# Optimization experiments

Measured on AMD Instinct MI355X. Metric: run time of the kernel, lower is better.

## Reference

```python
import jax, jax.numpy as jnp
import numpy as np
import math

B, T, C, H = 2, 2048, 1024, 16
HD = C // H  # head_dim = 64
SCALE = 1.0 / math.sqrt(HD)


def _e8_head_dirs(n_heads: int) -> np.ndarray:
    # Type-1 E8 roots in original generation order: (+-1 at i, +-1 at j), i<j,
    # sign order (-1,-1),(-1,1),(1,-1),(1,1); then L2-normalized (norm sqrt(2)).
    roots = []
    for i in range(8):
        for j in range(i + 1, 8):
            for si in (-1.0, 1.0):
                for sj in (-1.0, 1.0):
                    r = np.zeros(8, dtype=np.float32)
                    r[i] = si
                    r[j] = sj
                    roots.append(r)
    roots = np.stack(roots)  # [112, 8], first n_heads used
    roots = roots / np.linalg.norm(roots, axis=1, keepdims=True)
    return roots[:n_heads]


def setup_inputs() -> dict:
    key = jax.random.key(0)
    k1, k2, k3, k4 = jax.random.split(key, 4)
    x = jax.random.normal(k1, (B, T, C), dtype=jnp.float32)
    # nn.Linear-style init scale
    w_qkv = jax.random.normal(k2, (C, 3 * C), dtype=jnp.float32) * (1.0 / math.sqrt(C))
    w_out = jax.random.normal(k3, (C, C), dtype=jnp.float32) * (1.0 / math.sqrt(C))
    head_scales = jax.random.normal(k4, (H,), dtype=jnp.float32) * 0.1
    head_dirs = jnp.asarray(_e8_head_dirs(H))  # [H, 8] buffer (not trained)
    return {"x": x, "w_qkv": w_qkv, "w_out": w_out,
            "head_scales": head_scales, "head_dirs": head_dirs}


def reference(x, w_qkv, w_out, head_scales, head_dirs):
    Bx, Tx, Cx = x.shape
    qkv = (x @ w_qkv).reshape(Bx, Tx, 3, H, HD)
    qkv = jnp.transpose(qkv, (2, 0, 3, 1, 4))  # [3, B, H, T, HD]
    q, k, v = qkv[0], qkv[1], qkv[2]
    scores = jnp.einsum('bhqd,bhkd->bhqk', q, k) * SCALE  # [B,H,T,T]
    causal = jnp.tril(jnp.ones((Tx, Tx), dtype=bool))
    scores = jnp.where(causal[None, None], scores, -jnp.inf)
    # E8 geometric bias: rank-1 per-head bias from projections onto root dirs
    q_proj = jnp.einsum('bhtd,hd->bht', q[..., :8], head_dirs)
    k_proj = jnp.einsum('bhtd,hd->bht', k[..., :8], head_dirs)
    geo_bias = q_proj[..., :, None] * k_proj[..., None, :]  # [B,H,T,T]
    scores = scores + head_scales[None, :, None, None] * geo_bias
    attn = jax.nn.softmax(scores, axis=-1)
    out = jnp.einsum('bhqk,bhkd->bhqd', attn, v)  # [B,H,T,HD]
    out = jnp.transpose(out, (0, 2, 1, 3)).reshape(Bx, Tx, Cx)
    return out @ w_out
```

## Files before the change

kernel.cpp:

```cpp
#include <hip/hip_runtime.h>
#include <stdint.h>


typedef float f32x4 __attribute__((ext_vector_type(4)));
typedef unsigned short u16x8 __attribute__((ext_vector_type(8)));
typedef unsigned short u16x4 __attribute__((ext_vector_type(4)));
typedef unsigned int u32x2 __attribute__((ext_vector_type(2)));
typedef __bf16 bf16x8 __attribute__((ext_vector_type(8)));

static __device__ __forceinline__ unsigned short f2bf(float f) {
  unsigned u = __float_as_uint(f);
  u += 0x7FFFu + ((u >> 16) & 1u);
  return (unsigned short)(u >> 16);
}
static __device__ __forceinline__ float bf2f(unsigned short s) {
  return __uint_as_float(((unsigned)s) << 16);
}
static __device__ __forceinline__ f32x4 mfma16(u16x8 a, u16x8 b, f32x4 c) {
  return __builtin_amdgcn_mfma_f32_16x16x32_bf16(
      __builtin_bit_cast(bf16x8, a), __builtin_bit_cast(bf16x8, b), c, 0, 0, 0);
}
static __device__ __forceinline__ unsigned cvtpk(float lo, float hi) {
  unsigned d;
  asm("v_cvt_pk_bf16_f32 %0, %1, %2" : "=v"(d) : "v"(lo), "v"(hi));
  return d;
}

#define GLD16(gp, lp) __builtin_amdgcn_global_load_lds( \
    (const __attribute__((address_space(1))) unsigned int*)(gp), \
    (__attribute__((address_space(3))) unsigned int*)(lp), 16, 0, 0)

__global__ __launch_bounds__(256) void k_cast(const float* __restrict__ in,
                                              unsigned short* __restrict__ out, int n4) {
  int i = blockIdx.x * 256 + threadIdx.x;
  if (i >= n4) return;
  f32x4 v = *(const f32x4*)(in + (size_t)i * 4);
  u16x4 o;
#pragma unroll
  for (int j = 0; j < 4; ++j) o[j] = f2bf(v[j]);
  *(u16x4*)(out + (size_t)i * 4) = o;
}

__global__ __launch_bounds__(256) void k_transpose(const float* __restrict__ in,
                                                   unsigned short* __restrict__ out,
                                                   int R, int Cc) {
  __shared__ float t[64][65];
  int tr = blockIdx.y * 64, tc = blockIdx.x * 64;
  int tx = threadIdx.x & 15, ty = threadIdx.x >> 4;
#pragma unroll
  for (int i = 0; i < 4; ++i) {
    int rr = ty + i * 16;
    f32x4 v = *(const f32x4*)(in + (size_t)(tr + rr) * Cc + tc + tx * 4);
#pragma unroll
    for (int j = 0; j < 4; ++j) t[rr][tx * 4 + j] = v[j];
  }
  __syncthreads();
#pragma unroll
  for (int i = 0; i < 4; ++i) {
    int cc = ty + i * 16;
    int rr = tx * 4;
    u16x4 o;
#pragma unroll
    for (int j = 0; j < 4; ++j) o[j] = f2bf(t[rr + j][cc]);
    *(u16x4*)(out + (size_t)(tc + cc) * R + tr + rr) = o;
  }
}

template <int MODE>
__global__ __launch_bounds__(256) void k_gemm(const unsigned short* __restrict__ A,
                                              const unsigned short* __restrict__ Bt,
                                              unsigned short* __restrict__ qo,
                                              unsigned short* __restrict__ ko,
                                              unsigned short* __restrict__ vTo,
                                              float* __restrict__ fo) {
  __shared__ unsigned short lA[128 * 32];
  __shared__ unsigned short lB[128 * 32];
  const int tid = threadIdx.x;
  const int lane = tid & 63, wid = tid >> 6;
  const int wr = wid >> 1, wc = wid & 1;
  const int r = lane & 15, g = lane >> 4;
  const int mbase = blockIdx.y * 128;
  const int nbase = blockIdx.x * 128;

  f32x4 acc[4][4] = {};

  for (int kt = 0; kt < 32; ++kt) {
    __syncthreads();
#pragma unroll
    for (int p = 0; p < 2; ++p) {
      int L = p * 4096 + tid * 16;
      int row = L >> 6;
      int blk = (L >> 4) & 3;
      GLD16(A + (size_t)(mbase + row) * 1024 + kt * 32 + blk * 8, lA + (L >> 1));
      GLD16(Bt + (size_t)(nbase + row) * 1024 + kt * 32 + blk * 8, lB + (L >> 1));
    }
    __syncthreads();
    u16x8 af[4], bfv[4];
#pragma unroll
    for (int m = 0; m < 4; ++m)
      af[m] = *(const u16x8*)(lA + (wr * 64 + m * 16 + r) * 32 + g * 8);
#pragma unroll
    for (int n = 0; n < 4; ++n)
      bfv[n] = *(const u16x8*)(lB + (wc * 64 + n * 16 + r) * 32 + g * 8);
#pragma unroll
    for (int m = 0; m < 4; ++m)
#pragma unroll
      for (int n = 0; n < 4; ++n) acc[m][n] = mfma16(af[m], bfv[n], acc[m][n]);
  }

#pragma unroll
  for (int m = 0; m < 4; ++m) {
#pragma unroll
    for (int n = 0; n < 4; ++n) {
      int ng = nbase + wc * 64 + n * 16 + r;
      int m0 = mbase + wr * 64 + m * 16 + g * 4;
      if (MODE == 0) {
        int sec = ng >> 10, rem = ng & 1023, hh = rem >> 6, d = rem & 63;
        int b = m0 >> 11, t0 = m0 & 2047;
        size_t bh = (size_t)(b * 16 + hh);
        if (sec == 2) {
          u16x4 o;
#pragma unroll
          for (int e = 0; e < 4; ++e) o[e] = f2bf(acc[m][n][e]);
          *(u16x4*)(vTo + (bh * 64 + d) * 2048 + t0) = o;
        } else {
          unsigned short* dst = (sec == 0 ? qo : ko);
#pragma unroll
          for (int e = 0; e < 4; ++e)
            dst[(bh * 2048 + t0 + e) * 64 + d] = f2bf(acc[m][n][e]);
        }
      } else {
#pragma unroll
        for (int e = 0; e < 4; ++e)
          fo[(size_t)(m0 + e) * 1024 + ng] = acc[m][n][e];
      }
    }
  }
}

__global__ __launch_bounds__(256) void k_attn(const unsigned short* __restrict__ qb,
                                              const unsigned short* __restrict__ kb,
                                              const unsigned short* __restrict__ vTb,
                                              const float* __restrict__ hsc,
                                              const float* __restrict__ hdir,
                                              unsigned short* __restrict__ o2) {
  __shared__ unsigned short lK[2][64 * 64];
  __shared__ unsigned short lV[2][64 * 64];
  __shared__ unsigned short lP[4][16 * 64];

  const int tid = threadIdx.x, lane = tid & 63, wid = tid >> 6;
  const int r = lane & 15, g = lane >> 4;
  const int bid = blockIdx.x;
  const int u = bid & 255, kq = bid >> 8;
  const int bh = u & 31, j = u >> 5;
  const int a = (kq == 0) ? j : (kq == 1) ? (31 - j) : (kq == 2) ? (8 + j) : (23 - j);
  const int nk = a + 1;
  const int qbase = a * 64;
  const int h = bh & 15, bi = bh >> 4;

  const size_t kbase = (size_t)bh * (2048 * 64);
  const size_t vbase = (size_t)bh * (64 * 2048);

  auto STAGE = [&](int buf, int kt) {
    unsigned short* dK = (unsigned short*)lK[buf];
    unsigned short* dV = (unsigned short*)lV[buf];
#pragma unroll
    for (int p = 0; p < 2; ++p) {
      int L = p * 4096 + tid * 16;
      int row = L >> 7;
      int cb = (L >> 4) & 7;
      int cbg = cb ^ (row & 7);
      GLD16(kb + kbase + (size_t)(kt * 64 + row) * 64 + cbg * 8, dK + (L >> 1));
      GLD16(vTb + vbase + (size_t)row * 2048 + kt * 64 + cbg * 8, dV + (L >> 1));
    }
  };

  STAGE(0, 0);

  const float LOG2E = 1.44269504088896f;
  const float hs = hsc[h];
  float dir8[8];
#pragma unroll
  for (int j2 = 0; j2 < 8; ++j2) dir8[j2] = hdir[h * 8 + j2];

  u16x8 qc0, qc1;
  {
    const unsigned short* qrow = qb + ((size_t)bh * 2048 + qbase + wid * 16 + r) * 64;
    float proj = 0.f;
    u16x8 qv = *(const u16x8*)qrow;
#pragma unroll
    for (int j2 = 0; j2 < 8; ++j2) proj += bf2f(qv[j2]) * dir8[j2];
#pragma unroll
    for (int s = 0; s < 2; ++s) {
      u16x8 raw = *(const u16x8*)(qrow + s * 32 + g * 8);
      u16x8 ov;
#pragma unroll
      for (int j2 = 0; j2 < 8; ++j2) {
        float v = bf2f(raw[j2]) * (0.125f * LOG2E);
        if (s == 0 && g == 0) v += (hs * LOG2E) * proj * dir8[j2];
        ov[j2] = f2bf(v);
      }
      if (s == 0) qc0 = ov; else qc1 = ov;
    }
  }

  f32x4 accO[4] = {};
  float mrow = -1e30f, lp = 0.f;
  unsigned short* pw = &lP[wid][0];
  const int swz = (r & 7) << 4;
  const int qq = qbase + wid * 16 + r;

  for (int kt = 0; kt < nk; ++kt) {
    asm volatile("s_waitcnt lgkmcnt(0)" ::: "memory");
    __builtin_amdgcn_sched_barrier(0);
    __builtin_amdgcn_s_barrier();
    __builtin_amdgcn_sched_barrier(0);

    if (kt + 1 < nk) STAGE((kt + 1) & 1, kt + 1);

    if (kt + 1 < nk) {
      asm volatile("s_waitcnt vmcnt(4)" ::: "memory");
    } else {
      asm volatile("s_waitcnt vmcnt(0)" ::: "memory");
    }
    __builtin_amdgcn_sched_barrier(0);
    __builtin_amdgcn_s_barrier();
    __builtin_amdgcn_sched_barrier(0);

    const char* lKc = (const char*)lK[kt & 1];
    const char* lVc = (const char*)lV[kt & 1];

    f32x4 accS[4];
    __builtin_amdgcn_s_setprio(1);
#pragma unroll
    for (int ct = 0; ct < 4; ++ct) {
      f32x4 s4 = {0.f, 0.f, 0.f, 0.f};
      int krow = ct * 16 + r;
      int sw = (krow & 7) << 4;
      u16x8 kf0 = *(const u16x8*)(lKc + krow * 128 + ((g * 16) ^ sw));
      u16x8 kf1 = *(const u16x8*)(lKc + krow * 128 + ((64 + g * 16) ^ sw));
      s4 = mfma16(kf0, qc0, s4);
      s4 = mfma16(kf1, qc1, s4);
      accS[ct] = s4;
    }
    __builtin_amdgcn_s_setprio(0);

    if (kt == nk - 1) {
#pragma unroll
      for (int ct = 0; ct < 4; ++ct)
#pragma unroll
        for (int e = 0; e < 4; ++e) {
          int kk = kt * 64 + ct * 16 + g * 4 + e;
          if (kk > qq) accS[ct][e] = -1e30f;
        }
    }

    float pm;
    {
      float t0 = fmaxf(fmaxf(accS[0][0], accS[0][1]), fmaxf(accS[0][2], accS[0][3]));
      float t1 = fmaxf(fmaxf(accS[1][0], accS[1][1]), fmaxf(accS[1][2], accS[1][3]));
      float t2 = fmaxf(fmaxf(accS[2][0], accS[2][1]), fmaxf(accS[2][2], accS[2][3]));
      float t3 = fmaxf(fmaxf(accS[3][0], accS[3][1]), fmaxf(accS[3][2], accS[3][3]));
      pm = fmaxf(fmaxf(t0, t1), fmaxf(t2, t3));
    }
    if (__any(pm > mrow + 8.f)) {
      float v = pm;
      v = fmaxf(v, __shfl_xor(v, 16, 64));
      v = fmaxf(v, __shfl_xor(v, 32, 64));
      float mn = fmaxf(mrow, v);
      float al = exp2f(mrow - mn);
#pragma unroll
      for (int dt = 0; dt < 4; ++dt)
#pragma unroll
        for (int e = 0; e < 4; ++e) accO[dt][e] *= al;
      lp *= al;
      mrow = mn;
    }

    float p[4][4];
#pragma unroll
    for (int ct = 0; ct < 4; ++ct)
#pragma unroll
      for (int e = 0; e < 4; ++e) p[ct][e] = exp2f(accS[ct][e] - mrow);
#pragma unroll
    for (int ct = 0; ct < 4; ++ct)
      lp += (p[ct][0] + p[ct][1]) + (p[ct][2] + p[ct][3]);

#pragma unroll
    for (int ct = 0; ct < 4; ++ct) {
      u32x2 w;
      w[0] = cvtpk(p[ct][0], p[ct][1]);
      w[1] = cvtpk(p[ct][2], p[ct][3]);
      *(u32x2*)((char*)pw + r * 128 + ((ct * 32 + g * 8) ^ swz)) = w;
    }
    asm volatile("s_waitcnt lgkmcnt(0)" ::: "memory");
    __builtin_amdgcn_sched_barrier(0);

    __builtin_amdgcn_s_setprio(1);
#pragma unroll
    for (int s = 0; s < 2; ++s) {
      u16x8 pa = *(const u16x8*)((const char*)pw + r * 128 + ((s * 64 + g * 16) ^ swz));
#pragma unroll
      for (int dt = 0; dt < 4; ++dt) {
        int dd = dt * 16 + r;
        u16x8 vf = *(const u16x8*)(lVc + dd * 128 + ((s * 64 + g * 16) ^ ((dd & 7) << 4)));
        accO[dt] = mfma16(vf, pa, accO[dt]);
      }
    }
    __builtin_amdgcn_s_setprio(0);
  }

  lp += __shfl_xor(lp, 16, 64);
  lp += __shfl_xor(lp, 32, 64);
  float inv = 1.f / lp;
#pragma unroll
  for (int dt = 0; dt < 4; ++dt) {
    u16x4 o;
#pragma unroll
    for (int e = 0; e < 4; ++e) o[e] = f2bf(accO[dt][e] * inv);
    *(u16x4*)(o2 + ((size_t)(bi * 2048 + qq)) * 1024 + h * 64 + dt * 16 + g * 4) = o;
  }
}

extern "C" void kernel_launch(void* const* d_in, const int* in_sizes, int n_in,
                              void* d_out, int out_size, void* d_ws, size_t ws_size,
                              hipStream_t stream) {
  const float* x    = (const float*)d_in[0];
  const float* wqkv = (const float*)d_in[1];
  const float* wout = (const float*)d_in[2];
  const float* hsc  = (const float*)d_in[3];
  const float* hdir = (const float*)d_in[4];
  float* outp = (float*)d_out;

  char* ws = (char*)d_ws;
  unsigned short* xb    = (unsigned short*)(ws + 0);
  unsigned short* wqkvT = (unsigned short*)(ws + 8388608);
  unsigned short* woutT = (unsigned short*)(ws + 14680064);
  unsigned short* qb    = (unsigned short*)(ws + 16777216);
  unsigned short* kb    = (unsigned short*)(ws + 25165824);
  unsigned short* vT    = (unsigned short*)(ws + 33554432);
  unsigned short* x2b   = (unsigned short*)(ws + 41943040);
  if (ws_size < 50331648u) return;

  k_cast<<<4096, 256, 0, stream>>>(x, xb, 1048576);
  k_transpose<<<dim3(48, 16), 256, 0, stream>>>(wqkv, wqkvT, 1024, 3072);
  k_transpose<<<dim3(16, 16), 256, 0, stream>>>(wout, woutT, 1024, 1024);
  k_gemm<0><<<dim3(24, 32), 256, 0, stream>>>(xb, wqkvT, qb, kb, vT, nullptr);
  k_attn<<<dim3(1024), 256, 0, stream>>>(qb, kb, vT, hsc, hdir, x2b);
  k_gemm<1><<<dim3(8, 32), 256, 0, stream>>>(x2b, woutT, nullptr, nullptr, nullptr, outp);
}
```

Before: 119.4 us.

## Process 128 query rows per attention block and fuse prep kernels

The attention kernel now handles two 64-row query tiles per block. Each wave holds two 16-row query fragments and reuses every staged K/V tile for both, which halves the K/V global loads and LDS staging per query row. Blocks are paired front and back for causal balance, and the grid drops to 512 blocks with launch_bounds set to 2 blocks per SM. The cast kernel and the two transpose kernels are merged into one launch to cut launch overhead. The cost is higher register pressure and fewer blocks in flight.

```diff
diff --git a/kernel.cpp b/kernel.cpp
--- a/kernel.cpp
+++ b/kernel.cpp
@@ -30,22 +30,37 @@
     (const __attribute__((address_space(1))) unsigned int*)(gp), \
     (__attribute__((address_space(3))) unsigned int*)(lp), 16, 0, 0)
 
-__global__ __launch_bounds__(256) void k_cast(const float* __restrict__ in,
-                                              unsigned short* __restrict__ out, int n4) {
-  int i = blockIdx.x * 256 + threadIdx.x;
-  if (i >= n4) return;
-  f32x4 v = *(const f32x4*)(in + (size_t)i * 4);
-  u16x4 o;
-#pragma unroll
-  for (int j = 0; j < 4; ++j) o[j] = f2bf(v[j]);
-  *(u16x4*)(out + (size_t)i * 4) = o;
-}
-
-__global__ __launch_bounds__(256) void k_transpose(const float* __restrict__ in,
-                                                   unsigned short* __restrict__ out,
-                                                   int R, int Cc) {
+__global__ __launch_bounds__(256) void k_prep(const float* __restrict__ x,
+                                              const float* __restrict__ wqkv,
+                                              const float* __restrict__ wout,
+                                              unsigned short* __restrict__ xb,
+                                              unsigned short* __restrict__ wqkvT,
+                                              unsigned short* __restrict__ woutT) {
   __shared__ float t[64][65];
-  int tr = blockIdx.y * 64, tc = blockIdx.x * 64;
+  const int bid = blockIdx.x;
+  if (bid < 4096) {
+    int i = bid * 256 + threadIdx.x;
+    f32x4 v = *(const f32x4*)(x + (size_t)i * 4);
+    u16x4 o;
+#pragma unroll
+    for (int j = 0; j < 4; ++j) o[j] = f2bf(v[j]);
+    *(u16x4*)(xb + (size_t)i * 4) = o;
+    return;
+  }
+  const float* in;
+  unsigned short* out;
+  int Cc, bx, by;
+  if (bid < 4864) {
+    int tt = bid - 4096;
+    in = wqkv; out = wqkvT; Cc = 3072;
+    bx = tt % 48; by = tt / 48;
+  } else {
+    int tt = bid - 4864;
+    in = wout; out = woutT; Cc = 1024;
+    bx = tt & 15; by = tt >> 4;
+  }
+  const int R = 1024;
+  int tr = by * 64, tc = bx * 64;
   int tx = threadIdx.x & 15, ty = threadIdx.x >> 4;
 #pragma unroll
   for (int i = 0; i < 4; ++i) {
@@ -138,24 +153,24 @@
   }
 }
 
-__global__ __launch_bounds__(256) void k_attn(const unsigned short* __restrict__ qb,
-                                              const unsigned short* __restrict__ kb,
-                                              const unsigned short* __restrict__ vTb,
-                                              const float* __restrict__ hsc,
-                                              const float* __restrict__ hdir,
-                                              unsigned short* __restrict__ o2) {
+__global__ __launch_bounds__(256, 2) void k_attn(const unsigned short* __restrict__ qb,
+                                                 const unsigned short* __restrict__ kb,
+                                                 const unsigned short* __restrict__ vTb,
+                                                 const float* __restrict__ hsc,
+                                                 const float* __restrict__ hdir,
+                                                 unsigned short* __restrict__ o2) {
   __shared__ unsigned short lK[2][64 * 64];
   __shared__ unsigned short lV[2][64 * 64];
-  __shared__ unsigned short lP[4][16 * 64];
+  __shared__ unsigned short lP[4][32 * 64];
 
   const int tid = threadIdx.x, lane = tid & 63, wid = tid >> 6;
   const int r = lane & 15, g = lane >> 4;
   const int bid = blockIdx.x;
   const int u = bid & 255, kq = bid >> 8;
   const int bh = u & 31, j = u >> 5;
-  const int a = (kq == 0) ? j : (kq == 1) ? (31 - j) : (kq == 2) ? (8 + j) : (23 - j);
-  const int nk = a + 1;
-  const int qbase = a * 64;
+  const int a = kq ? (15 - j) : j;
+  const int nk = 2 * a + 2;
+  const int qbase = a * 128;
   const int h = bh & 15, bi = bh >> 4;
 
   const size_t kbase = (size_t)bh * (2048 * 64);
@@ -183,9 +198,9 @@
 #pragma unroll
   for (int j2 = 0; j2 < 8; ++j2) dir8[j2] = hdir[h * 8 + j2];
 
-  u16x8 qc0, qc1;
-  {
-    const unsigned short* qrow = qb + ((size_t)bh * 2048 + qbase + wid * 16 + r) * 64;
+  u16x8 q0c0, q0c1, q1c0, q1c1;
+  auto QF = [&](int rowbase, u16x8& c0, u16x8& c1) {
+    const unsigned short* qrow = qb + ((size_t)bh * 2048 + rowbase + r) * 64;
     float proj = 0.f;
     u16x8 qv = *(const u16x8*)qrow;
 #pragma unroll
@@ -200,15 +215,18 @@
         if (s == 0 && g == 0) v += (hs * LOG2E) * proj * dir8[j2];
         ov[j2] = f2bf(v);
       }
-      if (s == 0) qc0 = ov; else qc1 = ov;
-    }
-  }
-
-  f32x4 accO[4] = {};
-  float mrow = -1e30f, lp = 0.f;
+      if (s == 0) c0 = ov; else c1 = ov;
+    }
+  };
+  QF(qbase + wid * 16, q0c0, q0c1);
+  QF(qbase + 64 + wid * 16, q1c0, q1c1);
+
+  f32x4 accO0[4] = {}, accO1[4] = {};
+  float m0 = -1e30f, lp0 = 0.f, m1 = -1e30f, lp1 = 0.f;
   unsigned short* pw = &lP[wid][0];
   const int swz = (r & 7) << 4;
-  const int qq = qbase + wid * 16 + r;
+  const int q0 = qbase + wid * 16 + r;
+  const int q1 = q0 + 64;
 
   for (int kt = 0; kt < nk; ++kt) {
     asm volatile("s_waitcnt lgkmcnt(0)" ::: "memory");
@@ -230,68 +248,113 @@
     const char* lKc = (const char*)lK[kt & 1];
     const char* lVc = (const char*)lV[kt & 1];
 
-    f32x4 accS[4];
+    const bool skip0 = (kt == nk - 1);
+
+    f32x4 s0[4], s1[4];
     __builtin_amdgcn_s_setprio(1);
 #pragma unroll
     for (int ct = 0; ct < 4; ++ct) {
-      f32x4 s4 = {0.f, 0.f, 0.f, 0.f};
       int krow = ct * 16 + r;
       int sw = (krow & 7) << 4;
       u16x8 kf0 = *(const u16x8*)(lKc + krow * 128 + ((g * 16) ^ sw));
       u16x8 kf1 = *(const u16x8*)(lKc + krow * 128 + ((64 + g * 16) ^ sw));
-      s4 = mfma16(kf0, qc0, s4);
-      s4 = mfma16(kf1, qc1, s4);
-      accS[ct] = s4;
+      f32x4 t1 = {0.f, 0.f, 0.f, 0.f};
+      t1 = mfma16(kf0, q1c0, t1);
+      t1 = mfma16(kf1, q1c1, t1);
+      s1[ct] = t1;
+      if (!skip0) {
+        f32x4 t0 = {0.f, 0.f, 0.f, 0.f};
+        t0 = mfma16(kf0, q0c0, t0);
+        t0 = mfma16(kf1, q0c1, t0);
+        s0[ct] = t0;
+      }
     }
     __builtin_amdgcn_s_setprio(0);
 
-    if (kt == nk - 1) {
+    if (kt == nk - 2 && !0) {
 #pragma unroll
       for (int ct = 0; ct < 4; ++ct)
 #pragma unroll
         for (int e = 0; e < 4; ++e) {
           int kk = kt * 64 + ct * 16 + g * 4 + e;
-          if (kk > qq) accS[ct][e] = -1e30f;
+          if (kk > q0) s0[ct][e] = -1e30f;
         }
     }
-
-    float pm;
+    if (kt == nk - 1) {
+#pragma unroll
+      for (int ct = 0; ct < 4; ++ct)
+#pragma unroll
+        for (int e = 0; e < 4; ++e) {
+          int kk = kt * 64 + ct * 16 + g * 4 + e;
+          if (kk > q1) s1[ct][e] = -1e30f;
+        }
+    }
+
+    float pm0 = -1e30f, pm1;
+    if (!skip0) {
+      float t0 = fmaxf(fmaxf(s0[0][0], s0[0][1]), fmaxf(s0[0][2], s0[0][3]));
+      float t1 = fmaxf(fmaxf(s0[1][0], s0[1][1]), fmaxf(s0[1][2], s0[1][3]));
+      float t2 = fmaxf(fmaxf(s0[2][0], s0[2][1]), fmaxf(s0[2][2], s0[2][3]));
+      float t3 = fmaxf(fmaxf(s0[3][0], s0[3][1]), fmaxf(s0[3][2], s0[3][3]));
+      pm0 = fmaxf(fmaxf(t0, t1), fmaxf(t2, t3));
+    }
     {
-      float t0 = fmaxf(fmaxf(accS[0][0], accS[0][1]), fmaxf(accS[0][2], accS[0][3]));
-      float t1 = fmaxf(fmaxf(accS[1][0], accS[1][1]), fmaxf(accS[1][2], accS[1][3]));
-      float t2 = fmaxf(fmaxf(accS[2][0], accS[2][1]), fmaxf(accS[2][2], accS[2][3]));
-      float t3 = fmaxf(fmaxf(accS[3][0], accS[3][1]), fmaxf(accS[3][2], accS[3][3]));
-      pm = fmaxf(fmaxf(t0, t1), fmaxf(t2, t3));
-    }
-    if (__any(pm > mrow + 8.f)) {
-      float v = pm;
-      v = fmaxf(v, __shfl_xor(v, 16, 64));
-      v = fmaxf(v, __shfl_xor(v, 32, 64));
-      float mn = fmaxf(mrow, v);
-      float al = exp2f(mrow - mn);
-#pragma unroll
-      for (int dt = 0; dt < 4; ++dt)
-#pragma unroll
-        for (int e = 0; e < 4; ++e) accO[dt][e] *= al;
-      lp *= al;
-      mrow = mn;
-    }
-
-    float p[4][4];
-#pragma unroll
-    for (int ct = 0; ct < 4; ++ct)
-#pragma unroll
-      for (int e = 0; e < 4; ++e) p[ct][e] = exp2f(accS[ct][e] - mrow);
-#pragma unroll
-    for (int ct = 0; ct < 4; ++ct)
-      lp += (p[ct][0] + p[ct][1]) + (p[ct][2] + p[ct][3]);
-
+      float t0 = fmaxf(fmaxf(s1[0][0], s1[0][1]), fmaxf(s1[0][2], s1[0][3]));
+      float t1 = fmaxf(fmaxf(s1[1][0], s1[1][1]), fmaxf(s1[1][2], s1[1][3]));
+      float t2 = fmaxf(fmaxf(s1[2][0], s1[2][1]), fmaxf(s1[2][2], s1[2][3]));
+      float t3 = fmaxf(fmaxf(s1[3][0], s1[3][1]), fmaxf(s1[3][2], s1[3][3]));
+      pm1 = fmaxf(fmaxf(t0, t1), fmaxf(t2, t3));
+    }
+    if (__any((pm0 > m0 + 8.f) | (pm1 > m1 + 8.f))) {
+      if (!skip0) {
+        float v = pm0;
+        v = fmaxf(v, __shfl_xor(v, 16, 64));
+        v = fmaxf(v, __shfl_xor(v, 32, 64));
+        float mn = fmaxf(m0, v);
+        float al = exp2f(m0 - mn);
+#pragma unroll
+        for (int dt = 0; dt < 4; ++dt)
+#pragma unroll
+          for (int e = 0; e < 4; ++e) accO0[dt][e] *= al;
+        lp0 *= al;
+        m0 = mn;
+      }
+      {
+        float v = pm1;
+        v = fmaxf(v, __shfl_xor(v, 16, 64));
+        v = fmaxf(v, __shfl_xor(v, 32, 64));
+        float mn = fmaxf(m1, v);
+        float al = exp2f(m1 - mn);
+#pragma unroll
+        for (int dt = 0; dt < 4; ++dt)
+#pragma unroll
+          for (int e = 0; e < 4; ++e) accO1[dt][e] *= al;
+        lp1 *= al;
+        m1 = mn;
+      }
+    }
+
+    if (!skip0) {
+#pragma unroll
+      for (int ct = 0; ct < 4; ++ct) {
+        float p0 = exp2f(s0[ct][0] - m0), p1 = exp2f(s0[ct][1] - m0);
+        float p2 = exp2f(s0[ct][2] - m0), p3 = exp2f(s0[ct][3] - m0);
+        lp0 += (p0 + p1) + (p2 + p3);
+        u32x2 w;
+        w[0] = cvtpk(p0, p1);
+        w[1] = cvtpk(p2, p3);
+        *(u32x2*)((char*)pw + r * 128 + ((ct * 32 + g * 8) ^ swz)) = w;
+      }
+    }
 #pragma unroll
     for (int ct = 0; ct < 4; ++ct) {
+      float p0 = exp2f(s1[ct][0] - m1), p1 = exp2f(s1[ct][1] - m1);
+      float p2 = exp2f(s1[ct][2] - m1), p3 = exp2f(s1[ct][3] - m1);
+      lp1 += (p0 + p1) + (p2 + p3);
       u32x2 w;
-      w[0] = cvtpk(p[ct][0], p[ct][1]);
-      w[1] = cvtpk(p[ct][2], p[ct][3]);
-      *(u32x2*)((char*)pw + r * 128 + ((ct * 32 + g * 8) ^ swz)) = w;
+      w[0] = cvtpk(p0, p1);
+      w[1] = cvtpk(p2, p3);
+      *(u32x2*)((char*)pw + (16 + r) * 128 + ((ct * 32 + g * 8) ^ swz)) = w;
     }
     asm volatile("s_waitcnt lgkmcnt(0)" ::: "memory");
     __builtin_amdgcn_sched_barrier(0);
@@ -299,26 +362,36 @@
     __builtin_amdgcn_s_setprio(1);
 #pragma unroll
     for (int s = 0; s < 2; ++s) {
-      u16x8 pa = *(const u16x8*)((const char*)pw + r * 128 + ((s * 64 + g * 16) ^ swz));
+      u16x8 pa1 = *(const u16x8*)((const char*)pw + (16 + r) * 128 + ((s * 64 + g * 16) ^ swz));
+      u16x8 pa0;
+      if (!skip0)
+        pa0 = *(const u16x8*)((const char*)pw + r * 128 + ((s * 64 + g * 16) ^ swz));
 #pragma unroll
       for (int dt = 0; dt < 4; ++dt) {
         int dd = dt * 16 + r;
         u16x8 vf = *(const u16x8*)(lVc + dd * 128 + ((s * 64 + g * 16) ^ ((dd & 7) << 4)));
-        accO[dt] = mfma16(vf, pa, accO[dt]);
+        accO1[dt] = mfma16(vf, pa1, accO1[dt]);
+        if (!skip0) accO0[dt] = mfma16(vf, pa0, accO0[dt]);
       }
     }
     __builtin_amdgcn_s_setprio(0);
   }
 
-  lp += __shfl_xor(lp, 16, 64);
-  lp += __shfl_xor(lp, 32, 64);
-  float inv = 1.f / lp;
+  lp0 += __shfl_xor(lp0, 16, 64);
+  lp0 += __shfl_xor(lp0, 32, 64);
+  lp1 += __shfl_xor(lp1, 16, 64);
+  lp1 += __shfl_xor(lp1, 32, 64);
+  float inv0 = 1.f / lp0, inv1 = 1.f / lp1;
 #pragma unroll
   for (int dt = 0; dt < 4; ++dt) {
-    u16x4 o;
-#pragma unroll
-    for (int e = 0; e < 4; ++e) o[e] = f2bf(accO[dt][e] * inv);
-    *(u16x4*)(o2 + ((size_t)(bi * 2048 + qq)) * 1024 + h * 64 + dt * 16 + g * 4) = o;
+    u16x4 o0, o1;
+#pragma unroll
+    for (int e = 0; e < 4; ++e) {
+      o0[e] = f2bf(accO0[dt][e] * inv0);
+      o1[e] = f2bf(accO1[dt][e] * inv1);
+    }
+    *(u16x4*)(o2 + ((size_t)(bi * 2048 + q0)) * 1024 + h * 64 + dt * 16 + g * 4) = o0;
+    *(u16x4*)(o2 + ((size_t)(bi * 2048 + q1)) * 1024 + h * 64 + dt * 16 + g * 4) = o1;
   }
 }
 
@@ -342,10 +415,8 @@
   unsigned short* x2b   = (unsigned short*)(ws + 41943040);
   if (ws_size < 50331648u) return;
 
-  k_cast<<<4096, 256, 0, stream>>>(x, xb, 1048576);
-  k_transpose<<<dim3(48, 16), 256, 0, stream>>>(wqkv, wqkvT, 1024, 3072);
-  k_transpose<<<dim3(16, 16), 256, 0, stream>>>(wout, woutT, 1024, 1024);
+  k_prep<<<5120, 256, 0, stream>>>(x, wqkv, wout, xb, wqkvT, woutT);
   k_gemm<0><<<dim3(24, 32), 256, 0, stream>>>(xb, wqkvT, qb, kb, vT, nullptr);
-  k_attn<<<dim3(1024), 256, 0, stream>>>(qb, kb, vT, hsc, hdir, x2b);
+  k_attn<<<dim3(512), 256, 0, stream>>>(qb, kb, vT, hsc, hdir, x2b);
   k_gemm<1><<<dim3(8, 32), 256, 0, stream>>>(x2b, woutT, nullptr, nullptr, nullptr, outp);
 }
```

Measured after the change: 127.4 us. 6.7% more time.

## Pair causal query tiles per attention block and merge prep kernels

Applied to the files above, without the earlier changes.

The attention kernel now uses 128-thread blocks that each own two 32-row query tiles taken from opposite ends of the causal triangle (pr and 63-pr). A block runs a fixed 33 KV iterations, switching the softmax state and Q fragments after the first tile's diagonal, so every block does the same amount of work. The three preprocessing kernels (x cast and the two weight transposes) are merged into one launch to cut launch overhead. The cost is more loads per thread in each KV stage, deeper vmcnt waits, and two waves per block instead of four.

```diff
diff --git a/kernel.cpp b/kernel.cpp
--- a/kernel.cpp
+++ b/kernel.cpp
@@ -30,22 +30,37 @@
     (const __attribute__((address_space(1))) unsigned int*)(gp), \
     (__attribute__((address_space(3))) unsigned int*)(lp), 16, 0, 0)
 
-__global__ __launch_bounds__(256) void k_cast(const float* __restrict__ in,
-                                              unsigned short* __restrict__ out, int n4) {
-  int i = blockIdx.x * 256 + threadIdx.x;
-  if (i >= n4) return;
-  f32x4 v = *(const f32x4*)(in + (size_t)i * 4);
-  u16x4 o;
-#pragma unroll
-  for (int j = 0; j < 4; ++j) o[j] = f2bf(v[j]);
-  *(u16x4*)(out + (size_t)i * 4) = o;
-}
-
-__global__ __launch_bounds__(256) void k_transpose(const float* __restrict__ in,
-                                                   unsigned short* __restrict__ out,
-                                                   int R, int Cc) {
+__global__ __launch_bounds__(256) void k_prep(const float* __restrict__ x,
+                                              const float* __restrict__ wqkv,
+                                              const float* __restrict__ wout,
+                                              unsigned short* __restrict__ xb,
+                                              unsigned short* __restrict__ wqkvT,
+                                              unsigned short* __restrict__ woutT) {
   __shared__ float t[64][65];
-  int tr = blockIdx.y * 64, tc = blockIdx.x * 64;
+  const int bid = blockIdx.x;
+  if (bid < 4096) {
+    int i = bid * 256 + threadIdx.x;
+    f32x4 v = *(const f32x4*)(x + (size_t)i * 4);
+    u16x4 o;
+#pragma unroll
+    for (int j = 0; j < 4; ++j) o[j] = f2bf(v[j]);
+    *(u16x4*)(xb + (size_t)i * 4) = o;
+    return;
+  }
+  const float* in;
+  unsigned short* out;
+  int Cc, bx, by;
+  if (bid < 4864) {
+    int tt = bid - 4096;
+    in = wqkv; out = wqkvT; Cc = 3072;
+    bx = tt % 48; by = tt / 48;
+  } else {
+    int tt = bid - 4864;
+    in = wout; out = woutT; Cc = 1024;
+    bx = tt & 15; by = tt >> 4;
+  }
+  const int R = 1024;
+  int tr = by * 64, tc = bx * 64;
   int tx = threadIdx.x & 15, ty = threadIdx.x >> 4;
 #pragma unroll
   for (int i = 0; i < 4; ++i) {
@@ -138,24 +153,23 @@
   }
 }
 
-__global__ __launch_bounds__(256) void k_attn(const unsigned short* __restrict__ qb,
-                                              const unsigned short* __restrict__ kb,
-                                              const unsigned short* __restrict__ vTb,
-                                              const float* __restrict__ hsc,
-                                              const float* __restrict__ hdir,
-                                              unsigned short* __restrict__ o2) {
+__global__ __launch_bounds__(128, 2) void k_attn(const unsigned short* __restrict__ qb,
+                                                 const unsigned short* __restrict__ kb,
+                                                 const unsigned short* __restrict__ vTb,
+                                                 const float* __restrict__ hsc,
+                                                 const float* __restrict__ hdir,
+                                                 unsigned short* __restrict__ o2) {
   __shared__ unsigned short lK[2][64 * 64];
   __shared__ unsigned short lV[2][64 * 64];
-  __shared__ unsigned short lP[4][16 * 64];
+  __shared__ unsigned short lP[2][16 * 64];
 
   const int tid = threadIdx.x, lane = tid & 63, wid = tid >> 6;
   const int r = lane & 15, g = lane >> 4;
   const int bid = blockIdx.x;
-  const int u = bid & 255, kq = bid >> 8;
-  const int bh = u & 31, j = u >> 5;
-  const int a = (kq == 0) ? j : (kq == 1) ? (31 - j) : (kq == 2) ? (8 + j) : (23 - j);
-  const int nk = a + 1;
-  const int qbase = a * 64;
+  const int bh = bid & 31;
+  const int pr = bid >> 5;
+  const int tA = pr, tB = 63 - pr;
+  const int nkA = (tA >> 1) + 1;
   const int h = bh & 15, bi = bh >> 4;
 
   const size_t kbase = (size_t)bh * (2048 * 64);
@@ -165,8 +179,8 @@
     unsigned short* dK = (unsigned short*)lK[buf];
     unsigned short* dV = (unsigned short*)lV[buf];
 #pragma unroll
-    for (int p = 0; p < 2; ++p) {
-      int L = p * 4096 + tid * 16;
+    for (int p = 0; p < 4; ++p) {
+      int L = p * 2048 + tid * 16;
       int row = L >> 7;
       int cb = (L >> 4) & 7;
       int cbg = cb ^ (row & 7);
@@ -183,9 +197,9 @@
 #pragma unroll
   for (int j2 = 0; j2 < 8; ++j2) dir8[j2] = hdir[h * 8 + j2];
 
-  u16x8 qc0, qc1;
-  {
-    const unsigned short* qrow = qb + ((size_t)bh * 2048 + qbase + wid * 16 + r) * 64;
+  u16x8 qAc0, qAc1, qBc0, qBc1;
+  auto QF = [&](int rowbase, u16x8& c0, u16x8& c1) {
+    const unsigned short* qrow = qb + ((size_t)bh * 2048 + rowbase + r) * 64;
     float proj = 0.f;
     u16x8 qv = *(const u16x8*)qrow;
 #pragma unroll
@@ -200,26 +214,34 @@
         if (s == 0 && g == 0) v += (hs * LOG2E) * proj * dir8[j2];
         ov[j2] = f2bf(v);
       }
-      if (s == 0) qc0 = ov; else qc1 = ov;
-    }
-  }
+      if (s == 0) c0 = ov; else c1 = ov;
+    }
+  };
+  QF(tA * 32 + wid * 16, qAc0, qAc1);
+  QF(tB * 32 + wid * 16, qBc0, qBc1);
 
   f32x4 accO[4] = {};
   float mrow = -1e30f, lp = 0.f;
+  u16x8 qc0 = qAc0, qc1 = qAc1;
+  int qq = tA * 32 + wid * 16 + r;
   unsigned short* pw = &lP[wid][0];
   const int swz = (r & 7) << 4;
-  const int qq = qbase + wid * 16 + r;
-
-  for (int kt = 0; kt < nk; ++kt) {
+
+  for (int it = 0; it < 33; ++it) {
+    const int kt = (it < nkA) ? it : it - nkA;
+
     asm volatile("s_waitcnt lgkmcnt(0)" ::: "memory");
     __builtin_amdgcn_sched_barrier(0);
     __builtin_amdgcn_s_barrier();
     __builtin_amdgcn_sched_barrier(0);
 
-    if (kt + 1 < nk) STAGE((kt + 1) & 1, kt + 1);
-
-    if (kt + 1 < nk) {
-      asm volatile("s_waitcnt vmcnt(4)" ::: "memory");
+    if (it + 1 < 33) {
+      int nt = it + 1;
+      STAGE(nt & 1, (nt < nkA) ? nt : nt - nkA);
+    }
+
+    if (it + 1 < 33) {
+      asm volatile("s_waitcnt vmcnt(8)" ::: "memory");
     } else {
       asm volatile("s_waitcnt vmcnt(0)" ::: "memory");
     }
@@ -227,8 +249,8 @@
     __builtin_amdgcn_s_barrier();
     __builtin_amdgcn_sched_barrier(0);
 
-    const char* lKc = (const char*)lK[kt & 1];
-    const char* lVc = (const char*)lV[kt & 1];
+    const char* lKc = (const char*)lK[it & 1];
+    const char* lVc = (const char*)lV[it & 1];
 
     f32x4 accS[4];
     __builtin_amdgcn_s_setprio(1);
@@ -245,7 +267,8 @@
     }
     __builtin_amdgcn_s_setprio(0);
 
-    if (kt == nk - 1) {
+    const bool diag = (it == nkA - 1) || (it == 32);
+    if (diag) {
 #pragma unroll
       for (int ct = 0; ct < 4; ++ct)
 #pragma unroll
@@ -308,17 +331,27 @@
       }
     }
     __builtin_amdgcn_s_setprio(0);
-  }
-
-  lp += __shfl_xor(lp, 16, 64);
-  lp += __shfl_xor(lp, 32, 64);
-  float inv = 1.f / lp;
-#pragma unroll
-  for (int dt = 0; dt < 4; ++dt) {
-    u16x4 o;
-#pragma unroll
-    for (int e = 0; e < 4; ++e) o[e] = f2bf(accO[dt][e] * inv);
-    *(u16x4*)(o2 + ((size_t)(bi * 2048 + qq)) * 1024 + h * 64 + dt * 16 + g * 4) = o;
+
+    if (diag) {
+      float ls = lp;
+      ls += __shfl_xor(ls, 16, 64);
+      ls += __shfl_xor(ls, 32, 64);
+      float inv = 1.f / ls;
+#pragma unroll
+      for (int dt = 0; dt < 4; ++dt) {
+        u16x4 o;
+#pragma unroll
+        for (int e = 0; e < 4; ++e) o[e] = f2bf(accO[dt][e] * inv);
+        *(u16x4*)(o2 + ((size_t)(bi * 2048 + qq)) * 1024 + h * 64 + dt * 16 + g * 4) = o;
+      }
+      if (it == nkA - 1 && it != 32) {
+#pragma unroll
+        for (int dt = 0; dt < 4; ++dt) accO[dt] = (f32x4){0.f, 0.f, 0.f, 0.f};
+        mrow = -1e30f; lp = 0.f;
+        qq = tB * 32 + wid * 16 + r;
+        qc0 = qBc0; qc1 = qBc1;
+      }
+    }
   }
 }
 
@@ -342,10 +375,8 @@
   unsigned short* x2b   = (unsigned short*)(ws + 41943040);
   if (ws_size < 50331648u) return;
 
-  k_cast<<<4096, 256, 0, stream>>>(x, xb, 1048576);
-  k_transpose<<<dim3(48, 16), 256, 0, stream>>>(wqkv, wqkvT, 1024, 3072);
-  k_transpose<<<dim3(16, 16), 256, 0, stream>>>(wout, woutT, 1024, 1024);
+  k_prep<<<5120, 256, 0, stream>>>(x, wqkv, wout, xb, wqkvT, woutT);
   k_gemm<0><<<dim3(24, 32), 256, 0, stream>>>(xb, wqkvT, qb, kb, vT, nullptr);
-  k_attn<<<dim3(1024), 256, 0, stream>>>(qb, kb, vT, hsc, hdir, x2b);
+  k_attn<<<dim3(1024), 128, 0, stream>>>(qb, kb, vT, hsc, hdir, x2b);
   k_gemm<1><<<dim3(8, 32), 256, 0, stream>>>(x2b, woutT, nullptr, nullptr, nullptr, outp);
 }
```

Measured after the change: 121.8 us. 2.1% more time.
